# Performance work log

Hardware: AMD Instinct MI355X
Metric: run time of the kernel (lower is better)

Reference implementation:

```python
import jax, jax.numpy as jnp
import numpy as np
from jax import lax

C_CLIP = 10.0
TEMP = 1.0
NEG = 1e8


def setup_inputs() -> dict:
    key = jax.random.key(0)
    ks = jax.random.split(key, 20)
    B, N, H, M = 16, 1000, 128, 2
    s = 0.08
    inp = {
        "enc_h": jax.random.normal(ks[0], (B, N, H), jnp.float32),
        "mask0": jnp.zeros((B, N), jnp.float32),
        "Wq1": jax.random.normal(ks[1], (M, 2 * H, H), jnp.float32) * s,
        "Wref1": jax.random.normal(ks[2], (M, H, H), jnp.float32) * s,
        "Vec1": jax.random.normal(ks[3], (M, H, H), jnp.float32) * s,
        "Wq3": jax.random.normal(ks[4], (M, H, H), jnp.float32) * s,
        "Wref3": jax.random.normal(ks[5], (M, H, H), jnp.float32) * s,
        "Vec3": jax.random.normal(ks[6], (M, H, H), jnp.float32) * s,
        "Wq4": jax.random.normal(ks[7], (M, H, H), jnp.float32) * s,
        "Wref4": jax.random.normal(ks[8], (M, H, H), jnp.float32) * s,
        "Vec4": jax.random.normal(ks[9], (M, H, H), jnp.float32) * s,
        "Wmh": jax.random.normal(ks[10], (M * H, H), jnp.float32) * s,
        "Wq2": jax.random.normal(ks[11], (H, H), jnp.float32) * s,
        "Wref2": jax.random.normal(ks[12], (H, H), jnp.float32) * s,
        "Vec2": jax.random.normal(ks[13], (H,), jnp.float32) * s,
        "dec_inp": jax.random.normal(ks[14], (H,), jnp.float32) * s,
        "n_decode": 16,
    }
    return inp


def reference(enc_h, mask0, Wq1, Wref1, Vec1, Wq3, Wref3, Vec3,
              Wq4, Wref4, Vec4, Wmh, Wq2, Wref2, Vec2, dec_inp, n_decode):
    B, N, H = enc_h.shape
    ref = enc_h
    h_mean = ref.mean(axis=1)  # [B,H] graph embedding (encoder mean)
    # Precompute per-head reference projections (hoisted out of decode loop)
    r1 = jnp.einsum('bnd,mdh->bmnh', ref, Wref1)
    v1 = jnp.einsum('bnd,mdh->bmnh', ref, Vec1)
    r3 = jnp.einsum('bnd,mdh->bmnh', ref, Wref3)
    v3 = jnp.einsum('bnd,mdh->bmnh', ref, Vec3)
    r4 = jnp.einsum('bnd,mdh->bmnh', ref, Wref4)
    v4 = jnp.einsum('bnd,mdh->bmnh', ref, Vec4)
    r2 = ref @ Wref2  # [B,N,H]

    def glimpse(query, Wq, r, v, mask):
        # query: [B,Din]; r,v: [B,M,N,H]; mask: [B,N] (1 = unavailable)
        q = jnp.einsum('bi,mih->bmh', query, Wq)
        u = jnp.tanh(q[:, :, None, :] + r)              # [B,M,N,H]
        s = jnp.einsum('bmnh,bmnh->bmn', u, v)          # additive scores
        s = C_CLIP * jnp.tanh(s)                        # logit clipping
        s = s - NEG * mask[:, None, :]
        a = jax.nn.softmax(s, axis=-1)                  # [B,M,N]
        g = jnp.einsum('bmn,bmnh->bmh', a, r)           # per-head glimpse
        return g.reshape(B, -1) @ Wmh                   # merge heads -> [B,H]

    def step(carry, _):
        mask, prev = carry
        q0 = jnp.concatenate([h_mean, prev], axis=-1)   # [B,2H]
        q = glimpse(q0, Wq1, r1, v1, mask)
        q = glimpse(q, Wq3, r3, v3, mask)
        q = glimpse(q, Wq4, r4, v4, mask)
        # pointer logits: Vec2 . tanh(W_q2 q + W_ref2 ref)
        u = jnp.einsum('h,bnh->bn', Vec2, jnp.tanh((q @ Wq2)[:, None, :] + r2))
        u = C_CLIP * jnp.tanh(u)
        u = u - NEG * mask
        logp = jax.nn.log_softmax(u / TEMP, axis=-1)    # [B,N]
        sel = jnp.argmax(logp, axis=-1)                 # greedy job selection
        mask = mask.at[jnp.arange(B), sel].set(1.0)
        prev = jnp.take_along_axis(ref, sel[:, None, None], axis=1)[:, 0]
        return (mask, prev), (logp, sel)

    prev0 = jnp.broadcast_to(dec_inp, (B, H))
    (_, _), (logps, sels) = lax.scan(step, (mask0, prev0), None, length=n_decode)
    return logps, sels
```

## Files before the change

kernel.cpp:

```cpp
#include <hip/hip_runtime.h>


#define Bb 16
#define Nn 1000
#define Hh 128
#define Ss 16
#define TPB 1024
#define NW 16
#define NB 16
#define ROWS 63
#define TPT (Nn * Bb * Hh)

#define PPART(par, g, c, m) \
  ((((size_t)(par)*16 + (size_t)(g))*NB + (size_t)(c))*2 + (size_t)(m))*132
#define ABUF(buf, g) (((size_t)(buf)*16 + (size_t)(g)) * 272)

typedef float f32x4 __attribute__((ext_vector_type(4)));
#define NTL(p) __builtin_nontemporal_load((const f32x4*)(p))

__device__ __forceinline__ void red5_2(float& a, float& b) {
#pragma unroll
  for (int m = 1; m <= 16; m <<= 1) {
    a += __shfl_xor(a, m, 64);
    b += __shfl_xor(b, m, 64);
  }
}
__device__ __forceinline__ void red5_4(float& a, float& b, float& c, float& d) {
#pragma unroll
  for (int m = 1; m <= 16; m <<= 1) {
    a += __shfl_xor(a, m, 64);
    b += __shfl_xor(b, m, 64);
    c += __shfl_xor(c, m, 64);
    d += __shfl_xor(d, m, 64);
  }
}

__device__ __forceinline__ float tanh_fast(float x) {
  const float xc = fminf(fmaxf(x, -10.f), 10.f);
  const float e = __expf(xc + xc);
  return (e - 1.f) * __builtin_amdgcn_rcpf(e + 1.f);
}
__device__ __forceinline__ float dot4t(const f32x4 q, const f32x4 r, const f32x4 v) {
  return tanh_fast(q[0] + r[0]) * v[0] + tanh_fast(q[1] + r[1]) * v[1] +
         tanh_fast(q[2] + r[2]) * v[2] + tanh_fast(q[3] + r[3]) * v[3];
}

__device__ __forceinline__ float aload(const float* p) {
  return __hip_atomic_load(p, __ATOMIC_RELAXED, __HIP_MEMORY_SCOPE_AGENT);
}
__device__ __forceinline__ void astore(float* p, float v) {
  __hip_atomic_store(p, v, __ATOMIC_RELAXED, __HIP_MEMORY_SCOPE_AGENT);
}

__device__ __forceinline__ void gbar(int* fl, int c, int p, int tid, int lane) {
  __syncthreads();
  if (tid < 64) {
    if (lane == 0)
      __hip_atomic_store(&fl[c * 32], p, __ATOMIC_RELEASE, __HIP_MEMORY_SCOPE_AGENT);
    int v = p;
    while (true) {
      if (lane < NB)
        v = __hip_atomic_load(&fl[lane * 32], __ATOMIC_RELAXED, __HIP_MEMORY_SCOPE_AGENT);
      if (__all(v >= p)) break;
    }
  }
  __syncthreads();
}

__global__ __launch_bounds__(256) void ptr1_proj_kernel(
    const float* __restrict__ enc,
    const float* __restrict__ Wref1, const float* __restrict__ Vec1,
    const float* __restrict__ Wref3, const float* __restrict__ Vec3,
    const float* __restrict__ Wref4, const float* __restrict__ Vec4,
    const float* __restrict__ Wref2,
    float* __restrict__ outp) {
  __shared__ float At[128][64];
  __shared__ float Bs[128][64];
  const int rt = blockIdx.x;
  const int wy = blockIdx.y;
  const int mat = wy >> 1;
  const int ch = wy & 1;
  const int tid = threadIdx.x;

  const float* W;
  switch (mat >> 1) {
    case 0: W = Wref1; break;
    case 1: W = Vec1;  break;
    case 2: W = Wref3; break;
    case 3: W = Vec3;  break;
    case 4: W = Wref4; break;
    case 5: W = Vec4;  break;
    default: W = Wref2; break;
  }
  if (mat < 12) W += (size_t)(mat & 1) * (128 * 128);

  const float* asrc = enc + (size_t)rt * 64 * 128;
  for (int f = tid; f < 64 * 32; f += 256) {
    const int r = f >> 5, k4 = (f & 31) << 2;
    const float4 v = *(const float4*)(asrc + (size_t)r * 128 + k4);
    At[k4 + 0][r] = v.x; At[k4 + 1][r] = v.y;
    At[k4 + 2][r] = v.z; At[k4 + 3][r] = v.w;
  }
  for (int f = tid; f < 128 * 16; f += 256) {
    const int k = f >> 4, c4 = (f & 15) << 2;
    *(float4*)&Bs[k][c4] = *(const float4*)(W + (size_t)k * 128 + ch * 64 + c4);
  }
  __syncthreads();

  const int tx = tid & 15, ty = tid >> 4;
  float acc[4][4] = {{0.f}};
  for (int k = 0; k < 128; ++k) {
    const float4 a = *(const float4*)&At[k][ty * 4];
    const float4 b = *(const float4*)&Bs[k][tx * 4];
    acc[0][0] += a.x * b.x; acc[0][1] += a.x * b.y; acc[0][2] += a.x * b.z; acc[0][3] += a.x * b.w;
    acc[1][0] += a.y * b.x; acc[1][1] += a.y * b.y; acc[1][2] += a.y * b.z; acc[1][3] += a.y * b.w;
    acc[2][0] += a.z * b.x; acc[2][1] += a.z * b.y; acc[2][2] += a.z * b.z; acc[2][3] += a.z * b.w;
    acc[3][0] += a.w * b.x; acc[3][1] += a.w * b.y; acc[3][2] += a.w * b.z; acc[3][3] += a.w * b.w;
  }
  float* dst = outp + (size_t)mat * TPT + ((size_t)rt * 64 + ty * 4) * 128 + ch * 64 + tx * 4;
  for (int i = 0; i < 4; ++i) {
    float4 v; v.x = acc[i][0]; v.y = acc[i][1]; v.z = acc[i][2]; v.w = acc[i][3];
    *(float4*)(dst + (size_t)i * 128) = v;
  }
}

__global__ __launch_bounds__(1024, 4) void ptr1_decode_kernel(
    const float* __restrict__ enc, const float* __restrict__ mask0,
    const float* __restrict__ Wq1, const float* __restrict__ Wq3,
    const float* __restrict__ Wq4, const float* __restrict__ Wmh,
    const float* __restrict__ Wq2, const float* __restrict__ Vec2,
    const float* __restrict__ dec_inp, const float* __restrict__ proj,
    float* __restrict__ partials, float* __restrict__ accum,
    int* __restrict__ flags, float* __restrict__ out) {
  const int g = blockIdx.x & 15;
  const int c = blockIdx.x >> 4;
  const int tid = threadIdx.x;
  const int wv = tid >> 6;
  const int lane = tid & 63;
  const int half = lane >> 5;
  const int hl = lane & 31;
  const int h0 = hl << 2;
  const int start = c * ROWS;
  const int cnt = min(ROWS, Nn - start);
  const int jrow = wv * 2 + half;
  const int j2 = jrow + 32;
  const bool a2 = j2 < cnt;
  const int j2c = a2 ? j2 : jrow;
  int* fl = flags + g * (16 * 32);

  __shared__ float Wmh_lds[256 * 128];
  __shared__ __align__(16) float hmean[128];
  __shared__ __align__(16) float qprev[128];
  __shared__ __align__(16) float qcur[128];
  __shared__ __align__(16) float base1[256];
  __shared__ __align__(16) float qm[2][128];
  __shared__ __align__(16) float gfraw[256];
  __shared__ __align__(16) float vecl[128];
  __shared__ __align__(16) float wpart[NW][2][132];
  __shared__ __align__(16) float qpart[4][256];
  __shared__ __align__(16) float mpart[8][128];
  __shared__ float sS[2];
  __shared__ float maskl[64];
  __shared__ float ulocal[64];
  __shared__ int sel_sh;
  __shared__ float logZ_sh;

  {
    float4* wl = (float4*)Wmh_lds;
    const float4* wg = (const float4*)Wmh;
#pragma unroll
    for (int k = 0; k < 8; ++k) wl[tid + k * TPB] = wg[tid + k * TPB];
  }
  if (tid < 128) vecl[tid] = Vec2[tid];
  for (int j = tid; j < cnt; j += TPB) maskl[j] = mask0[(size_t)g * Nn + start + j];

  const size_t o1 = (size_t)jrow * Hh;
  const size_t o2 = (size_t)j2c * Hh;
  const size_t rowb = ((size_t)g * Nn + start) * Hh + h0;
  const float* pb = proj + rowb;

  {
    const float* eb = enc + rowb;
    const float4 eA = *(const float4*)(eb + o1);
    const float4 eB = *(const float4*)(eb + o2);
    float4 a;
    a.x = eA.x + (a2 ? eB.x : 0.f); a.y = eA.y + (a2 ? eB.y : 0.f);
    a.z = eA.z + (a2 ? eB.z : 0.f); a.w = eA.w + (a2 ? eB.w : 0.f);
    a.x += __shfl_xor(a.x, 32, 64); a.y += __shfl_xor(a.y, 32, 64);
    a.z += __shfl_xor(a.z, 32, 64); a.w += __shfl_xor(a.w, 32, 64);
    if (half == 0) *(float4*)&wpart[wv][0][4 + h0] = a;
    __syncthreads();
    if (tid < 128) {
      float s = 0.f;
      for (int w = 0; w < NW; ++w) s += wpart[w][0][4 + tid];
      astore(&partials[PPART(0, g, c, 0) + 4 + tid], s);
    }
    gbar(fl, c, 1, tid, lane);
    if (tid < 128) {
      float s = 0.f;
#pragma unroll 8
      for (int cc = 0; cc < NB; ++cc) s += aload(&partials[PPART(0, g, cc, 0) + 4 + tid]);
      hmean[tid] = s * (1.0f / (float)Nn);
    }
    if (tid >= 128 && tid < 256) qprev[tid - 128] = dec_inp[tid - 128];
    __syncthreads();
    {
      const int o = tid & 255, part = tid >> 8;
      const int m = o >> 7, h = o & 127;
      const float* wp = Wq1 + (size_t)m * 256 * 128 + (size_t)(part * 32) * 128 + h;
      const float* qc = hmean + part * 32;
      float acc = 0.f;
#pragma unroll 16
      for (int i = 0; i < 32; ++i) acc += qc[i] * wp[(size_t)i * 128];
      qpart[part][o] = acc;
    }
    __syncthreads();
    if (tid < 256)
      base1[tid] = qpart[0][tid] + qpart[1][tid] + qpart[2][tid] + qpart[3][tid];
    __syncthreads();
  }

  int p = 2;
  for (int step = 0; step < Ss; ++step) {
    for (int gl = 0; gl < 3; ++gl) {
      const float* r0p = pb + (size_t)(4 * gl + 0) * TPT;
      const float* r1p = pb + (size_t)(4 * gl + 1) * TPT;
      const float* v0p = pb + (size_t)(4 * gl + 2) * TPT;
      const float* v1p = pb + (size_t)(4 * gl + 3) * TPT;
      const f32x4 r0A = NTL(r0p + o1), r0B = NTL(r0p + o2);
      const f32x4 r1A = NTL(r1p + o1), r1B = NTL(r1p + o2);
      const f32x4 v0A = NTL(v0p + o1), v0B = NTL(v0p + o2);
      const f32x4 v1A = NTL(v1p + o1), v1B = NTL(v1p + o2);
      __builtin_amdgcn_sched_barrier(0);
      {
        const int o = tid & 255, part = tid >> 8;
        const int m = o >> 7, h = o & 127;
        const float* wp;
        const float* qc;
        if (gl == 0) {
          wp = Wq1 + (size_t)m * 256 * 128 + (size_t)(128 + part * 32) * 128 + h;
          qc = qprev + part * 32;
        } else {
          const float* Wq = (gl == 1) ? Wq3 : Wq4;
          wp = Wq + (size_t)m * 128 * 128 + (size_t)(part * 32) * 128 + h;
          qc = qcur + part * 32;
        }
        float acc = 0.f;
#pragma unroll 16
        for (int i = 0; i < 32; ++i) acc += qc[i] * wp[(size_t)i * 128];
        qpart[part][o] = acc;
      }
      __syncthreads();
      if (tid < 256) {
        float s = qpart[0][tid] + qpart[1][tid] + qpart[2][tid] + qpart[3][tid];
        if (gl == 0) s += base1[tid];
        (&qm[0][0])[tid] = s;
      }
      __syncthreads();

      const f32x4 qa = *(const f32x4*)&qm[0][h0];
      const f32x4 qb = *(const f32x4*)&qm[1][h0];
      const float mlA = maskl[jrow], mlB = maskl[j2c];
      float s0A = dot4t(qa, r0A, v0A), s1A = dot4t(qb, r1A, v1A);
      float s0B = dot4t(qa, r0B, v0B), s1B = dot4t(qb, r1B, v1B);
      red5_4(s0A, s1A, s0B, s1B);
      s0A = 10.f * tanh_fast(s0A) - 1e8f * mlA;
      s1A = 10.f * tanh_fast(s1A) - 1e8f * mlA;
      s0B = 10.f * tanh_fast(s0B) - 1e8f * mlB;
      s1B = 10.f * tanh_fast(s1B) - 1e8f * mlB;
      const float e0A = __expf(s0A - 10.f), e1A = __expf(s1A - 10.f);
      const float e0B = a2 ? __expf(s0B - 10.f) : 0.f;
      const float e1B = a2 ? __expf(s1B - 10.f) : 0.f;
      float S0 = e0A + e0B, S1 = e1A + e1B;
      f32x4 g0 = r0A * e0A + r0B * e0B;
      f32x4 g1 = r1A * e1A + r1B * e1B;
      S0 += __shfl_xor(S0, 32, 64); S1 += __shfl_xor(S1, 32, 64);
      g0[0] += __shfl_xor(g0[0], 32, 64); g0[1] += __shfl_xor(g0[1], 32, 64);
      g0[2] += __shfl_xor(g0[2], 32, 64); g0[3] += __shfl_xor(g0[3], 32, 64);
      g1[0] += __shfl_xor(g1[0], 32, 64); g1[1] += __shfl_xor(g1[1], 32, 64);
      g1[2] += __shfl_xor(g1[2], 32, 64); g1[3] += __shfl_xor(g1[3], 32, 64);
      if (half == 0) {
        *(f32x4*)&wpart[wv][0][4 + h0] = g0;
        *(f32x4*)&wpart[wv][1][4 + h0] = g1;
        if (hl == 0) { wpart[wv][0][0] = S0; wpart[wv][1][0] = S1; }
      }
      __syncthreads();
      float* ab = accum + ABUF(p & 3, g);
      float* zb = accum + ABUF((p + 1) & 3, g);
      if (tid < 256) {
        const int m = tid >> 7, h = tid & 127;
        float gs = 0.f;
        for (int w = 0; w < NW; ++w) gs += wpart[w][m][4 + h];
        unsafeAtomicAdd(&ab[m * 132 + 4 + h], gs);
        if (h == 0) {
          float ss = 0.f;
          for (int w = 0; w < NW; ++w) ss += wpart[w][m][0];
          unsafeAtomicAdd(&ab[m * 132], ss);
        }
      } else if (tid >= 512 && tid < 512 + 17) {
        const int idx = c * 17 + (tid - 512);
        if (idx < 272) astore(&zb[idx], 0.f);
      }
      gbar(fl, c, p, tid, lane);
      p++;
      if (tid < 256) gfraw[tid] = aload(&ab[(tid >> 7) * 132 + 4 + (tid & 127)]);
      if (tid >= 256 && tid < 258) sS[tid - 256] = aload(&ab[(tid - 256) * 132]);
      __syncthreads();
      {
        const int h = tid & 127, part = tid >> 7;
        const int m = part >> 2;
        float acc = 0.f;
        const float* wl = Wmh_lds + (size_t)part * 32 * 128 + h;
        const float* gg = gfraw + part * 32;
#pragma unroll 16
        for (int i = 0; i < 32; ++i) acc += gg[i] * wl[i * 128];
        mpart[part][h] = acc / sS[m];
      }
      __syncthreads();
      if (tid < 128) {
        float acc = 0.f;
        for (int w = 0; w < 8; ++w) acc += mpart[w][tid];
        qcur[tid] = acc;
      }
      __syncthreads();
    }

    const float* r2p = pb + (size_t)12 * TPT;
    const f32x4 rrA = NTL(r2p + o1);
    const f32x4 rrB = NTL(r2p + o2);
    __builtin_amdgcn_sched_barrier(0);
    {
      const int h = tid & 127, part = tid >> 7;
      float acc = 0.f;
      const float* wp = Wq2 + (size_t)part * 16 * 128 + h;
      const float* qc = qcur + part * 16;
#pragma unroll
      for (int i = 0; i < 16; ++i) acc += qc[i] * wp[(size_t)i * 128];
      mpart[part][h] = acc;
    }
    __syncthreads();
    if (tid < 128) {
      float acc = 0.f;
      for (int w = 0; w < 8; ++w) acc += mpart[w][tid];
      qm[0][tid] = acc;
    }
    __syncthreads();
    {
      const f32x4 q2 = *(const f32x4*)&qm[0][h0];
      const f32x4 vz = *(const f32x4*)&vecl[h0];
      float upA = dot4t(q2, rrA, vz);
      float upB = dot4t(q2, rrB, vz);
      red5_2(upA, upB);
      const float mlA = maskl[jrow], mlB = maskl[j2c];
      const float uA = 10.f * tanh_fast(upA) - 1e8f * mlA;
      const float uB = a2 ? (10.f * tanh_fast(upB) - 1e8f * mlB) : -3.0e38f;
      if (hl == 0) {
        ulocal[jrow] = uA;
        if (a2) ulocal[j2] = uB;
      }
      float Sv = __expf(uA - 10.f) + (a2 ? __expf(uB - 10.f) : 0.f);
      float um = uA; int ui = start + jrow;
      if (a2 && uB > um) { um = uB; ui = start + j2; }
      Sv += __shfl_xor(Sv, 32, 64);
      const float um2 = __shfl_xor(um, 32, 64);
      const int ui2 = __shfl_xor(ui, 32, 64);
      if (um2 > um || (um2 == um && ui2 < ui)) { um = um2; ui = ui2; }
      if (lane == 0) {
        wpart[wv][0][0] = Sv; wpart[wv][0][1] = um;
        wpart[wv][0][2] = __int_as_float(ui);
      }
    }
    __syncthreads();
    float* ab = accum + ABUF(p & 3, g);
    float* zb = accum + ABUF((p + 1) & 3, g);
    if (tid == 0) {
      float St = 0.f, bm = -3.0e38f; int bi = 0x7fffffff;
      for (int ww = 0; ww < NW; ++ww) {
        St += wpart[ww][0][0];
        const float m2 = wpart[ww][0][1];
        const int i2 = __float_as_int(wpart[ww][0][2]);
        if (m2 > bm || (m2 == bm && i2 < bi)) { bm = m2; bi = i2; }
      }
      unsigned ob = __float_as_uint(bm);
      ob = (ob & 0x80000000u) ? ~ob : (ob | 0x80000000u);
      const unsigned long long key =
          ((unsigned long long)ob << 32) | (0xFFFFFFFFu - (unsigned)bi);
      unsafeAtomicAdd(&ab[0], St);
      atomicMax((unsigned long long*)&ab[264], key);
    } else if (tid >= 512 && tid < 512 + 17) {
      const int idx = c * 17 + (tid - 512);
      if (idx < 272) astore(&zb[idx], 0.f);
    }
    gbar(fl, c, p, tid, lane);
    p++;
    if (tid == 0) {
      const float St = aload(&ab[0]);
      const unsigned long long key = __hip_atomic_load(
          (const unsigned long long*)&ab[264], __ATOMIC_RELAXED,
          __HIP_MEMORY_SCOPE_AGENT);
      sel_sh = (int)(0xFFFFFFFFu - (unsigned)(key & 0xFFFFFFFFu));
      logZ_sh = 10.f + __logf(St);
    }
    __syncthreads();
    const int sel = sel_sh;
    const float lz = logZ_sh;
    if (tid < 128)
      qprev[tid] = enc[((size_t)g * Nn + sel) * Hh + tid];
    for (int j = tid; j < cnt; j += TPB)
      out[(size_t)step * (Bb * Nn) + (size_t)g * Nn + start + j] = ulocal[j] - lz;
    if (c == 0 && tid == 0)
      out[(size_t)Ss * Bb * Nn + (size_t)step * Bb + g] = (float)sel;
    if (tid == 0 && sel >= start && sel < start + cnt) maskl[sel - start] = 1.0f;
    __syncthreads();
  }
}

extern "C" void kernel_launch(void* const* d_in, const int* in_sizes, int n_in,
                              void* d_out, int out_size, void* d_ws, size_t ws_size,
                              hipStream_t stream) {
  const float* enc     = (const float*)d_in[0];
  const float* mask0   = (const float*)d_in[1];
  const float* Wq1     = (const float*)d_in[2];
  const float* Wref1   = (const float*)d_in[3];
  const float* Vec1    = (const float*)d_in[4];
  const float* Wq3     = (const float*)d_in[5];
  const float* Wref3   = (const float*)d_in[6];
  const float* Vec3    = (const float*)d_in[7];
  const float* Wq4     = (const float*)d_in[8];
  const float* Wref4   = (const float*)d_in[9];
  const float* Vec4    = (const float*)d_in[10];
  const float* Wmh     = (const float*)d_in[11];
  const float* Wq2     = (const float*)d_in[12];
  const float* Wref2   = (const float*)d_in[13];
  const float* Vec2    = (const float*)d_in[14];
  const float* dec_inp = (const float*)d_in[15];
  float* out = (float*)d_out;

  char* ws = (char*)d_ws;
  int* flags      = (int*)ws;
  float* accum    = (float*)(ws + 32768);
  float* partials = (float*)(ws + 102400);
  float* proj     = (float*)(ws + 102400 + 540672);

  hipMemsetAsync(ws, 0, 102400, stream);

  dim3 pg(250, 26);
  ptr1_proj_kernel<<<pg, 256, 0, stream>>>(enc, Wref1, Vec1, Wref3, Vec3,
                                           Wref4, Vec4, Wref2, proj);

  void* args[] = {(void*)&enc,  (void*)&mask0, (void*)&Wq1, (void*)&Wq3,
                  (void*)&Wq4,  (void*)&Wmh,   (void*)&Wq2, (void*)&Vec2,
                  (void*)&dec_inp, (void*)&proj, (void*)&partials,
                  (void*)&accum, (void*)&flags, (void*)&out};
  hipLaunchCooperativeKernel((const void*)ptr1_decode_kernel, dim3(256),
                             dim3(1024), args, 0, stream);
}
```

Baseline: 943.5 us.

## Precompose Wmh with next-glimpse query weights and drop Wmh LDS staging

A new small kernel precomputes the products of Wmh with Wq3, Wq4 and Wq2, so each glimpse's head-merge and the next query projection collapse into one matvec against a precomposed matrix. This removes a separate matvec and block barrier per glimpse and frees the 128KB Wmh copy in LDS, which lowers shared-memory pressure in the cooperative decode kernel. The three glimpses are unrolled by hand. The composed matrices are read from global memory instead of LDS each step, and the changed summation order can slightly alter floating-point results.

```diff
diff --git a/kernel.cpp b/kernel.cpp
--- a/kernel.cpp
+++ b/kernel.cpp
@@ -11,9 +11,9 @@
 #define ROWS 63
 #define TPT (Nn * Bb * Hh)
 
-#define PPART(par, g, c, m) \
-  ((((size_t)(par)*16 + (size_t)(g))*NB + (size_t)(c))*2 + (size_t)(m))*132
+#define PPART(g, c) (((size_t)(g)*NB + (size_t)(c)) * 132)
 #define ABUF(buf, g) (((size_t)(buf)*16 + (size_t)(g)) * 272)
+#define CSLOT 32768
 
 typedef float f32x4 __attribute__((ext_vector_type(4)));
 #define NTL(p) __builtin_nontemporal_load((const f32x4*)(p))
@@ -34,7 +34,6 @@
     d += __shfl_xor(d, m, 64);
   }
 }
-
 __device__ __forceinline__ float tanh_fast(float x) {
   const float xc = fminf(fmaxf(x, -10.f), 10.f);
   const float e = __expf(xc + xc);
@@ -44,14 +43,12 @@
   return tanh_fast(q[0] + r[0]) * v[0] + tanh_fast(q[1] + r[1]) * v[1] +
          tanh_fast(q[2] + r[2]) * v[2] + tanh_fast(q[3] + r[3]) * v[3];
 }
-
 __device__ __forceinline__ float aload(const float* p) {
   return __hip_atomic_load(p, __ATOMIC_RELAXED, __HIP_MEMORY_SCOPE_AGENT);
 }
 __device__ __forceinline__ void astore(float* p, float v) {
   __hip_atomic_store(p, v, __ATOMIC_RELAXED, __HIP_MEMORY_SCOPE_AGENT);
 }
-
 __device__ __forceinline__ void gbar(int* fl, int c, int p, int tid, int lane) {
   __syncthreads();
   if (tid < 64) {
@@ -124,12 +121,57 @@
   }
 }
 
+__global__ __launch_bounds__(256) void ptr1_cmat_kernel(
+    const float* __restrict__ Wmh, const float* __restrict__ Wq3,
+    const float* __restrict__ Wq4, const float* __restrict__ Wq2,
+    float* __restrict__ cout) {
+  __shared__ float At[128][64];
+  __shared__ float Bs[128][64];
+  const int rt = blockIdx.x;
+  const int wy = blockIdx.y;
+  const int s = wy >> 1;
+  const int ch = wy & 1;
+  const int tid = threadIdx.x;
+
+  const float* W = (s < 2) ? (Wq3 + (size_t)(s & 1) * 16384)
+                 : (s < 4) ? (Wq4 + (size_t)((s - 2) & 1) * 16384)
+                           : Wq2;
+
+  const float* asrc = Wmh + (size_t)rt * 64 * 128;
+  for (int f = tid; f < 64 * 32; f += 256) {
+    const int r = f >> 5, k4 = (f & 31) << 2;
+    const float4 v = *(const float4*)(asrc + (size_t)r * 128 + k4);
+    At[k4 + 0][r] = v.x; At[k4 + 1][r] = v.y;
+    At[k4 + 2][r] = v.z; At[k4 + 3][r] = v.w;
+  }
+  for (int f = tid; f < 128 * 16; f += 256) {
+    const int k = f >> 4, c4 = (f & 15) << 2;
+    *(float4*)&Bs[k][c4] = *(const float4*)(W + (size_t)k * 128 + ch * 64 + c4);
+  }
+  __syncthreads();
+
+  const int tx = tid & 15, ty = tid >> 4;
+  float acc[4][4] = {{0.f}};
+  for (int k = 0; k < 128; ++k) {
+    const float4 a = *(const float4*)&At[k][ty * 4];
+    const float4 b = *(const float4*)&Bs[k][tx * 4];
+    acc[0][0] += a.x * b.x; acc[0][1] += a.x * b.y; acc[0][2] += a.x * b.z; acc[0][3] += a.x * b.w;
+    acc[1][0] += a.y * b.x; acc[1][1] += a.y * b.y; acc[1][2] += a.y * b.z; acc[1][3] += a.y * b.w;
+    acc[2][0] += a.z * b.x; acc[2][1] += a.z * b.y; acc[2][2] += a.z * b.z; acc[2][3] += a.z * b.w;
+    acc[3][0] += a.w * b.x; acc[3][1] += a.w * b.y; acc[3][2] += a.w * b.z; acc[3][3] += a.w * b.w;
+  }
+  float* dst = cout + (size_t)s * CSLOT + ((size_t)rt * 64 + ty * 4) * 128 + ch * 64 + tx * 4;
+  for (int i = 0; i < 4; ++i) {
+    float4 v; v.x = acc[i][0]; v.y = acc[i][1]; v.z = acc[i][2]; v.w = acc[i][3];
+    *(float4*)(dst + (size_t)i * 128) = v;
+  }
+}
+
 __global__ __launch_bounds__(1024, 4) void ptr1_decode_kernel(
     const float* __restrict__ enc, const float* __restrict__ mask0,
-    const float* __restrict__ Wq1, const float* __restrict__ Wq3,
-    const float* __restrict__ Wq4, const float* __restrict__ Wmh,
-    const float* __restrict__ Wq2, const float* __restrict__ Vec2,
-    const float* __restrict__ dec_inp, const float* __restrict__ proj,
+    const float* __restrict__ Wq1, const float* __restrict__ Wq2,
+    const float* __restrict__ Vec2, const float* __restrict__ dec_inp,
+    const float* __restrict__ proj, const float* __restrict__ cmat,
     float* __restrict__ partials, float* __restrict__ accum,
     int* __restrict__ flags, float* __restrict__ out) {
   const int g = blockIdx.x & 15;
@@ -148,10 +190,8 @@
   const int j2c = a2 ? j2 : jrow;
   int* fl = flags + g * (16 * 32);
 
-  __shared__ float Wmh_lds[256 * 128];
   __shared__ __align__(16) float hmean[128];
   __shared__ __align__(16) float qprev[128];
-  __shared__ __align__(16) float qcur[128];
   __shared__ __align__(16) float base1[256];
   __shared__ __align__(16) float qm[2][128];
   __shared__ __align__(16) float gfraw[256];
@@ -159,18 +199,12 @@
   __shared__ __align__(16) float wpart[NW][2][132];
   __shared__ __align__(16) float qpart[4][256];
   __shared__ __align__(16) float mpart[8][128];
-  __shared__ float sS[2];
   __shared__ float maskl[64];
   __shared__ float ulocal[64];
   __shared__ int sel_sh;
   __shared__ float logZ_sh;
 
-  {
-    float4* wl = (float4*)Wmh_lds;
-    const float4* wg = (const float4*)Wmh;
-#pragma unroll
-    for (int k = 0; k < 8; ++k) wl[tid + k * TPB] = wg[tid + k * TPB];
-  }
+  float* qmf = &qm[0][0];
   if (tid < 128) vecl[tid] = Vec2[tid];
   for (int j = tid; j < cnt; j += TPB) maskl[j] = mask0[(size_t)g * Nn + start + j];
 
@@ -178,6 +212,9 @@
   const size_t o2 = (size_t)j2c * Hh;
   const size_t rowb = ((size_t)g * Nn + start) * Hh + h0;
   const float* pb = proj + rowb;
+  const float* C3 = cmat;
+  const float* C4 = cmat + 2 * CSLOT;
+  const float* C2 = cmat + 4 * CSLOT;
 
   {
     const float* eb = enc + rowb;
@@ -193,13 +230,13 @@
     if (tid < 128) {
       float s = 0.f;
       for (int w = 0; w < NW; ++w) s += wpart[w][0][4 + tid];
-      astore(&partials[PPART(0, g, c, 0) + 4 + tid], s);
+      astore(&partials[PPART(g, c) + 4 + tid], s);
     }
     gbar(fl, c, 1, tid, lane);
     if (tid < 128) {
       float s = 0.f;
 #pragma unroll 8
-      for (int cc = 0; cc < NB; ++cc) s += aload(&partials[PPART(0, g, cc, 0) + 4 + tid]);
+      for (int cc = 0; cc < NB; ++cc) s += aload(&partials[PPART(g, cc) + 4 + tid]);
       hmean[tid] = s * (1.0f / (float)Nn);
     }
     if (tid >= 128 && tid < 256) qprev[tid - 128] = dec_inp[tid - 128];
@@ -222,40 +259,29 @@
 
   int p = 2;
   for (int step = 0; step < Ss; ++step) {
-    for (int gl = 0; gl < 3; ++gl) {
-      const float* r0p = pb + (size_t)(4 * gl + 0) * TPT;
-      const float* r1p = pb + (size_t)(4 * gl + 1) * TPT;
-      const float* v0p = pb + (size_t)(4 * gl + 2) * TPT;
-      const float* v1p = pb + (size_t)(4 * gl + 3) * TPT;
-      const f32x4 r0A = NTL(r0p + o1), r0B = NTL(r0p + o2);
-      const f32x4 r1A = NTL(r1p + o1), r1B = NTL(r1p + o2);
-      const f32x4 v0A = NTL(v0p + o1), v0B = NTL(v0p + o2);
-      const f32x4 v1A = NTL(v1p + o1), v1B = NTL(v1p + o2);
+    const float* r0pA = pb + (size_t)0 * TPT;
+    const float* r1pA = pb + (size_t)1 * TPT;
+    const float* v0pA = pb + (size_t)2 * TPT;
+    const float* v1pA = pb + (size_t)3 * TPT;
+    {
+      const f32x4 r0A = NTL(r0pA + o1), r0B = NTL(r0pA + o2);
+      const f32x4 r1A = NTL(r1pA + o1), r1B = NTL(r1pA + o2);
+      const f32x4 v0A = NTL(v0pA + o1), v0B = NTL(v0pA + o2);
+      const f32x4 v1A = NTL(v1pA + o1), v1B = NTL(v1pA + o2);
       __builtin_amdgcn_sched_barrier(0);
       {
         const int o = tid & 255, part = tid >> 8;
         const int m = o >> 7, h = o & 127;
-        const float* wp;
-        const float* qc;
-        if (gl == 0) {
-          wp = Wq1 + (size_t)m * 256 * 128 + (size_t)(128 + part * 32) * 128 + h;
-          qc = qprev + part * 32;
-        } else {
-          const float* Wq = (gl == 1) ? Wq3 : Wq4;
-          wp = Wq + (size_t)m * 128 * 128 + (size_t)(part * 32) * 128 + h;
-          qc = qcur + part * 32;
-        }
+        const float* wp = Wq1 + (size_t)m * 256 * 128 + (size_t)(128 + part * 32) * 128 + h;
+        const float* qc = qprev + part * 32;
         float acc = 0.f;
 #pragma unroll 16
         for (int i = 0; i < 32; ++i) acc += qc[i] * wp[(size_t)i * 128];
         qpart[part][o] = acc;
       }
       __syncthreads();
-      if (tid < 256) {
-        float s = qpart[0][tid] + qpart[1][tid] + qpart[2][tid] + qpart[3][tid];
-        if (gl == 0) s += base1[tid];
-        (&qm[0][0])[tid] = s;
-      }
+      if (tid < 256)
+        qmf[tid] = qpart[0][tid] + qpart[1][tid] + qpart[2][tid] + qpart[3][tid] + base1[tid];
       __syncthreads();
 
       const f32x4 qa = *(const f32x4*)&qm[0][h0];
@@ -297,45 +323,180 @@
           for (int w = 0; w < NW; ++w) ss += wpart[w][m][0];
           unsafeAtomicAdd(&ab[m * 132], ss);
         }
-      } else if (tid >= 512 && tid < 512 + 17) {
+      } else if (tid >= 512 && tid < 529) {
         const int idx = c * 17 + (tid - 512);
         if (idx < 272) astore(&zb[idx], 0.f);
       }
       gbar(fl, c, p, tid, lane);
       p++;
-      if (tid < 256) gfraw[tid] = aload(&ab[(tid >> 7) * 132 + 4 + (tid & 127)]);
-      if (tid >= 256 && tid < 258) sS[tid - 256] = aload(&ab[(tid - 256) * 132]);
-      __syncthreads();
-      {
-        const int h = tid & 127, part = tid >> 7;
-        const int m = part >> 2;
-        float acc = 0.f;
-        const float* wl = Wmh_lds + (size_t)part * 32 * 128 + h;
-        const float* gg = gfraw + part * 32;
+      if (tid < 256) {
+        const int mm = tid >> 7;
+        const float Sr = aload(&ab[mm * 132]);
+        gfraw[tid] = aload(&ab[mm * 132 + 4 + (tid & 127)]) / Sr;
+      }
+      __syncthreads();
+    }
+    {
+      const int o = tid & 255, part = tid >> 8;
+      const int m = o >> 7, h = o & 127;
+      const float* cp = C3 + (size_t)m * CSLOT + (size_t)(part * 64) * 128 + h;
+      const float* gc = gfraw + part * 64;
+      float acc = 0.f;
 #pragma unroll 16
-        for (int i = 0; i < 32; ++i) acc += gg[i] * wl[i * 128];
-        mpart[part][h] = acc / sS[m];
-      }
-      __syncthreads();
-      if (tid < 128) {
-        float acc = 0.f;
-        for (int w = 0; w < 8; ++w) acc += mpart[w][tid];
-        qcur[tid] = acc;
-      }
-      __syncthreads();
-    }
-
-    const float* r2p = pb + (size_t)12 * TPT;
-    const f32x4 rrA = NTL(r2p + o1);
-    const f32x4 rrB = NTL(r2p + o2);
-    __builtin_amdgcn_sched_barrier(0);
+      for (int i = 0; i < 64; ++i) acc += gc[i] * cp[(size_t)i * 128];
+      qpart[part][o] = acc;
+    }
+    __syncthreads();
+    if (tid < 256)
+      qmf[tid] = qpart[0][tid] + qpart[1][tid] + qpart[2][tid] + qpart[3][tid];
+    __syncthreads();
+
+    const float* r0pB = pb + (size_t)4 * TPT;
+    const float* r1pB = pb + (size_t)5 * TPT;
+    const float* v0pB = pb + (size_t)6 * TPT;
+    const float* v1pB = pb + (size_t)7 * TPT;
+    {
+      const f32x4 r0A = NTL(r0pB + o1), r0B = NTL(r0pB + o2);
+      const f32x4 r1A = NTL(r1pB + o1), r1B = NTL(r1pB + o2);
+      const f32x4 v0A = NTL(v0pB + o1), v0B = NTL(v0pB + o2);
+      const f32x4 v1A = NTL(v1pB + o1), v1B = NTL(v1pB + o2);
+      __builtin_amdgcn_sched_barrier(0);
+      const f32x4 qa = *(const f32x4*)&qm[0][h0];
+      const f32x4 qb = *(const f32x4*)&qm[1][h0];
+      const float mlA = maskl[jrow], mlB = maskl[j2c];
+      float s0A = dot4t(qa, r0A, v0A), s1A = dot4t(qb, r1A, v1A);
+      float s0B = dot4t(qa, r0B, v0B), s1B = dot4t(qb, r1B, v1B);
+      red5_4(s0A, s1A, s0B, s1B);
+      s0A = 10.f * tanh_fast(s0A) - 1e8f * mlA;
+      s1A = 10.f * tanh_fast(s1A) - 1e8f * mlA;
+      s0B = 10.f * tanh_fast(s0B) - 1e8f * mlB;
+      s1B = 10.f * tanh_fast(s1B) - 1e8f * mlB;
+      const float e0A = __expf(s0A - 10.f), e1A = __expf(s1A - 10.f);
+      const float e0B = a2 ? __expf(s0B - 10.f) : 0.f;
+      const float e1B = a2 ? __expf(s1B - 10.f) : 0.f;
+      float S0 = e0A + e0B, S1 = e1A + e1B;
+      f32x4 g0 = r0A * e0A + r0B * e0B;
+      f32x4 g1 = r1A * e1A + r1B * e1B;
+      S0 += __shfl_xor(S0, 32, 64); S1 += __shfl_xor(S1, 32, 64);
+      g0[0] += __shfl_xor(g0[0], 32, 64); g0[1] += __shfl_xor(g0[1], 32, 64);
+      g0[2] += __shfl_xor(g0[2], 32, 64); g0[3] += __shfl_xor(g0[3], 32, 64);
+      g1[0] += __shfl_xor(g1[0], 32, 64); g1[1] += __shfl_xor(g1[1], 32, 64);
+      g1[2] += __shfl_xor(g1[2], 32, 64); g1[3] += __shfl_xor(g1[3], 32, 64);
+      if (half == 0) {
+        *(f32x4*)&wpart[wv][0][4 + h0] = g0;
+        *(f32x4*)&wpart[wv][1][4 + h0] = g1;
+        if (hl == 0) { wpart[wv][0][0] = S0; wpart[wv][1][0] = S1; }
+      }
+      __syncthreads();
+      float* ab = accum + ABUF(p & 3, g);
+      float* zb = accum + ABUF((p + 1) & 3, g);
+      if (tid < 256) {
+        const int m = tid >> 7, h = tid & 127;
+        float gs = 0.f;
+        for (int w = 0; w < NW; ++w) gs += wpart[w][m][4 + h];
+        unsafeAtomicAdd(&ab[m * 132 + 4 + h], gs);
+        if (h == 0) {
+          float ss = 0.f;
+          for (int w = 0; w < NW; ++w) ss += wpart[w][m][0];
+          unsafeAtomicAdd(&ab[m * 132], ss);
+        }
+      } else if (tid >= 512 && tid < 529) {
+        const int idx = c * 17 + (tid - 512);
+        if (idx < 272) astore(&zb[idx], 0.f);
+      }
+      gbar(fl, c, p, tid, lane);
+      p++;
+      if (tid < 256) {
+        const int mm = tid >> 7;
+        const float Sr = aload(&ab[mm * 132]);
+        gfraw[tid] = aload(&ab[mm * 132 + 4 + (tid & 127)]) / Sr;
+      }
+      __syncthreads();
+    }
+    {
+      const int o = tid & 255, part = tid >> 8;
+      const int m = o >> 7, h = o & 127;
+      const float* cp = C4 + (size_t)m * CSLOT + (size_t)(part * 64) * 128 + h;
+      const float* gc = gfraw + part * 64;
+      float acc = 0.f;
+#pragma unroll 16
+      for (int i = 0; i < 64; ++i) acc += gc[i] * cp[(size_t)i * 128];
+      qpart[part][o] = acc;
+    }
+    __syncthreads();
+    if (tid < 256)
+      qmf[tid] = qpart[0][tid] + qpart[1][tid] + qpart[2][tid] + qpart[3][tid];
+    __syncthreads();
+
+    const float* r0pC = pb + (size_t)8 * TPT;
+    const float* r1pC = pb + (size_t)9 * TPT;
+    const float* v0pC = pb + (size_t)10 * TPT;
+    const float* v1pC = pb + (size_t)11 * TPT;
+    {
+      const f32x4 r0A = NTL(r0pC + o1), r0B = NTL(r0pC + o2);
+      const f32x4 r1A = NTL(r1pC + o1), r1B = NTL(r1pC + o2);
+      const f32x4 v0A = NTL(v0pC + o1), v0B = NTL(v0pC + o2);
+      const f32x4 v1A = NTL(v1pC + o1), v1B = NTL(v1pC + o2);
+      __builtin_amdgcn_sched_barrier(0);
+      const f32x4 qa = *(const f32x4*)&qm[0][h0];
+      const f32x4 qb = *(const f32x4*)&qm[1][h0];
+      const float mlA = maskl[jrow], mlB = maskl[j2c];
+      float s0A = dot4t(qa, r0A, v0A), s1A = dot4t(qb, r1A, v1A);
+      float s0B = dot4t(qa, r0B, v0B), s1B = dot4t(qb, r1B, v1B);
+      red5_4(s0A, s1A, s0B, s1B);
+      s0A = 10.f * tanh_fast(s0A) - 1e8f * mlA;
+      s1A = 10.f * tanh_fast(s1A) - 1e8f * mlA;
+      s0B = 10.f * tanh_fast(s0B) - 1e8f * mlB;
+      s1B = 10.f * tanh_fast(s1B) - 1e8f * mlB;
+      const float e0A = __expf(s0A - 10.f), e1A = __expf(s1A - 10.f);
+      const float e0B = a2 ? __expf(s0B - 10.f) : 0.f;
+      const float e1B = a2 ? __expf(s1B - 10.f) : 0.f;
+      float S0 = e0A + e0B, S1 = e1A + e1B;
+      f32x4 g0 = r0A * e0A + r0B * e0B;
+      f32x4 g1 = r1A * e1A + r1B * e1B;
+      S0 += __shfl_xor(S0, 32, 64); S1 += __shfl_xor(S1, 32, 64);
+      g0[0] += __shfl_xor(g0[0], 32, 64); g0[1] += __shfl_xor(g0[1], 32, 64);
+      g0[2] += __shfl_xor(g0[2], 32, 64); g0[3] += __shfl_xor(g0[3], 32, 64);
+      g1[0] += __shfl_xor(g1[0], 32, 64); g1[1] += __shfl_xor(g1[1], 32, 64);
+      g1[2] += __shfl_xor(g1[2], 32, 64); g1[3] += __shfl_xor(g1[3], 32, 64);
+      if (half == 0) {
+        *(f32x4*)&wpart[wv][0][4 + h0] = g0;
+        *(f32x4*)&wpart[wv][1][4 + h0] = g1;
+        if (hl == 0) { wpart[wv][0][0] = S0; wpart[wv][1][0] = S1; }
+      }
+      __syncthreads();
+      float* ab = accum + ABUF(p & 3, g);
+      float* zb = accum + ABUF((p + 1) & 3, g);
+      if (tid < 256) {
+        const int m = tid >> 7, h = tid & 127;
+        float gs = 0.f;
+        for (int w = 0; w < NW; ++w) gs += wpart[w][m][4 + h];
+        unsafeAtomicAdd(&ab[m * 132 + 4 + h], gs);
+        if (h == 0) {
+          float ss = 0.f;
+          for (int w = 0; w < NW; ++w) ss += wpart[w][m][0];
+          unsafeAtomicAdd(&ab[m * 132], ss);
+        }
+      } else if (tid >= 512 && tid < 529) {
+        const int idx = c * 17 + (tid - 512);
+        if (idx < 272) astore(&zb[idx], 0.f);
+      }
+      gbar(fl, c, p, tid, lane);
+      p++;
+      if (tid < 256) {
+        const int mm = tid >> 7;
+        const float Sr = aload(&ab[mm * 132]);
+        gfraw[tid] = aload(&ab[mm * 132 + 4 + (tid & 127)]) / Sr;
+      }
+      __syncthreads();
+    }
     {
       const int h = tid & 127, part = tid >> 7;
+      const float* cp = C2 + (size_t)(part * 32) * 128 + h;
+      const float* gc = gfraw + part * 32;
       float acc = 0.f;
-      const float* wp = Wq2 + (size_t)part * 16 * 128 + h;
-      const float* qc = qcur + part * 16;
-#pragma unroll
-      for (int i = 0; i < 16; ++i) acc += qc[i] * wp[(size_t)i * 128];
+#pragma unroll 16
+      for (int i = 0; i < 32; ++i) acc += gc[i] * cp[(size_t)i * 128];
       mpart[part][h] = acc;
     }
     __syncthreads();
@@ -345,7 +506,12 @@
       qm[0][tid] = acc;
     }
     __syncthreads();
-    {
+
+    const float* r2p = pb + (size_t)12 * TPT;
+    {
+      const f32x4 rrA = NTL(r2p + o1);
+      const f32x4 rrB = NTL(r2p + o2);
+      __builtin_amdgcn_sched_barrier(0);
       const f32x4 q2 = *(const f32x4*)&qm[0][h0];
       const f32x4 vz = *(const f32x4*)&vecl[h0];
       float upA = dot4t(q2, rrA, vz);
@@ -387,7 +553,7 @@
           ((unsigned long long)ob << 32) | (0xFFFFFFFFu - (unsigned)bi);
       unsafeAtomicAdd(&ab[0], St);
       atomicMax((unsigned long long*)&ab[264], key);
-    } else if (tid >= 512 && tid < 512 + 17) {
+    } else if (tid >= 512 && tid < 529) {
       const int idx = c * 17 + (tid - 512);
       if (idx < 272) astore(&zb[idx], 0.f);
     }
@@ -440,18 +606,19 @@
   int* flags      = (int*)ws;
   float* accum    = (float*)(ws + 32768);
   float* partials = (float*)(ws + 102400);
-  float* proj     = (float*)(ws + 102400 + 540672);
+  float* cmat     = (float*)(ws + 102400 + 135168);
+  float* proj     = (float*)(ws + 102400 + 135168 + 655360);
 
   hipMemsetAsync(ws, 0, 102400, stream);
 
   dim3 pg(250, 26);
   ptr1_proj_kernel<<<pg, 256, 0, stream>>>(enc, Wref1, Vec1, Wref3, Vec3,
                                            Wref4, Vec4, Wref2, proj);
-
-  void* args[] = {(void*)&enc,  (void*)&mask0, (void*)&Wq1, (void*)&Wq3,
-                  (void*)&Wq4,  (void*)&Wmh,   (void*)&Wq2, (void*)&Vec2,
-                  (void*)&dec_inp, (void*)&proj, (void*)&partials,
-                  (void*)&accum, (void*)&flags, (void*)&out};
+  ptr1_cmat_kernel<<<dim3(4, 10), 256, 0, stream>>>(Wmh, Wq3, Wq4, Wq2, cmat);
+
+  void* args[] = {(void*)&enc,  (void*)&mask0, (void*)&Wq1, (void*)&Wq2,
+                  (void*)&Vec2, (void*)&dec_inp, (void*)&proj, (void*)&cmat,
+                  (void*)&partials, (void*)&accum, (void*)&flags, (void*)&out};
   hipLaunchCooperativeKernel((const void*)ptr1_decode_kernel, dim3(256),
                              dim3(1024), args, 0, stream);
 }
```

Result: slower. 1.454 ms (+54.1%).
